# Kernel optimization log

Hardware: AMD Instinct MI355X
Metric: run time of the kernel (lower is better)

The kernel has to match this reference:

```python
import jax, jax.numpy as jnp
import numpy as np

N_NODES = 100000
NFEAT = 256
NHID = 8
HEADS = 8
NCLASS = 32
N_EDGES = 1600000
NEG_SLOPE = 0.2


def setup_inputs() -> dict:
    key = jax.random.key(0)
    ks = jax.random.split(key, 10)
    glorot = lambda k, shape: jax.random.uniform(
        k, shape, jnp.float32, -1.0, 1.0) * np.sqrt(6.0 / (shape[0] + shape[-1]))
    x = jax.random.normal(ks[0], (N_NODES, NFEAT), jnp.float32)
    edge_index = jax.random.randint(ks[1], (2, N_EDGES), 0, N_NODES, jnp.int64)
    W1 = glorot(ks[2], (NFEAT, HEADS * NHID))
    a_src1 = glorot(ks[3], (HEADS, NHID))
    a_dst1 = glorot(ks[4], (HEADS, NHID))
    b1 = jnp.zeros((HEADS * NHID,), jnp.float32)
    W2 = glorot(ks[5], (HEADS * NHID, NCLASS))
    a_src2 = glorot(ks[6], (1, NCLASS))
    a_dst2 = glorot(ks[7], (1, NCLASS))
    b2 = jnp.zeros((NCLASS,), jnp.float32)
    return {"x": x, "edge_index": edge_index, "W1": W1, "a_src1": a_src1,
            "a_dst1": a_dst1, "b1": b1, "W2": W2, "a_src2": a_src2,
            "a_dst2": a_dst2, "b2": b2}


def gat_conv(x, src, dst, W, a_src, a_dst, b, heads, ch, concat):
    """One PyG-style GATConv layer (eval mode, self-loops already in src/dst)."""
    n = x.shape[0]
    h = (x @ W).reshape(n, heads, ch)                      # [N,H,C]
    al_s = jnp.einsum('nhc,hc->nh', h, a_src)              # [N,H]
    al_d = jnp.einsum('nhc,hc->nh', h, a_dst)              # [N,H]
    e = al_s[src] + al_d[dst]                              # [E,H]
    e = jnp.where(e >= 0, e, NEG_SLOPE * e)                # LeakyReLU(0.2)
    # segment softmax over destination node (self-loops => no empty segments)
    m = jax.ops.segment_max(e, dst, num_segments=n)
    e = jnp.exp(e - m[dst])
    s = jax.ops.segment_sum(e, dst, num_segments=n)
    alpha = e / (s[dst] + 1e-16)                           # [E,H]
    msg = h[src] * alpha[:, :, None]                       # [E,H,C]
    out = jax.ops.segment_sum(msg, dst, num_segments=n)    # [N,H,C]
    out = out.reshape(n, heads * ch) if concat else out.mean(axis=1)
    return out + b


def reference(x, edge_index, W1, a_src1, a_dst1, b1, W2, a_src2, a_dst2, b2):
    n = x.shape[0]
    loop = jnp.arange(n, dtype=edge_index.dtype)
    src = jnp.concatenate([edge_index[0], loop])
    dst = jnp.concatenate([edge_index[1], loop])
    h = gat_conv(x, src, dst, W1, a_src1, a_dst1, b1, HEADS, NHID, True)
    h = jax.nn.elu(h)
    out = gat_conv(h, src, dst, W2, a_src2, a_dst2, b2, 1, NCLASS, False)
    return jax.nn.log_softmax(out, axis=1)
```

## Files before the change

kernel.cpp:

```cpp
#include <hip/hip_runtime.h>
#include <math.h>

#define N_NODES 100000
#define NFEAT 256
#define D1 64
#define HEADS 8
#define NHID 8
#define NCLASS 32
#define NUM_EDGES 1600000
#define E_TOT 1700000
#define NEG_SLOPE 0.2f

#define BSHIFT 8
#define NBUCK 391
#define BCAP 5120
#define BIN_EPB 4096
#define BIN_EPT 16
#define GEMM1_NB 1563


#define OFF_H1    0
#define OFF_H2    6400000
#define OFF_ALS1  12800000
#define OFF_ALD1  13600000
#define OFF_ALS2  14400000
#define OFF_ALD2  14500000
#define OFF_BCUR  14600000
#define OFF_ROWP  14601024
#define OFF_CNT   14701024
#define OFF_BIN   14801024
#define OFF_CSR   16802944

typedef __attribute__((ext_vector_type(8))) short bf16x8;
typedef __attribute__((ext_vector_type(4))) float f32x4;

__device__ __forceinline__ float lrelu(float x) { return x >= 0.f ? x : NEG_SLOPE * x; }
__device__ __forceinline__ float fast_elu(float x) { return x > 0.f ? x : __expf(x) - 1.f; }

__device__ __forceinline__ unsigned f32_to_bf16_rne(float f) {
    unsigned u = __float_as_uint(f);
    return (u + 0x7fffu + ((u >> 16) & 1u)) >> 16;
}
__device__ __forceinline__ unsigned pack_bf16x2(float lo, float hi) {
    return f32_to_bf16_rne(lo) | (f32_to_bf16_rne(hi) << 16);
}
__device__ __forceinline__ float2 unpack_bf16x2(unsigned v) {
    return make_float2(__uint_as_float(v << 16), __uint_as_float(v & 0xffff0000u));
}

__device__ __forceinline__ void edge_src_dst(const int* __restrict__ ei, int e, int& src, int& dst) {
    if (e < NUM_EDGES) { src = ei[e]; dst = ei[NUM_EDGES + e]; }
    else { src = e - NUM_EDGES; dst = e - NUM_EDGES; }
}

__global__ __launch_bounds__(256) void bin_kernel(const int* __restrict__ ei,
                                                  int* __restrict__ bcur,
                                                  int* __restrict__ bin) {
    __shared__ int lcnt[NBUCK];
    __shared__ int lbase[NBUCK];
    const int tid = threadIdx.x;
    for (int b = tid; b < NBUCK; b += 256) lcnt[b] = 0;
    __syncthreads();
    const int e0 = blockIdx.x * BIN_EPB;
    int pk[BIN_EPT], bk[BIN_EPT], loff[BIN_EPT];
#pragma unroll
    for (int i = 0; i < BIN_EPT; i++) {
        const int e = e0 + i * 256 + tid;
        if (e < E_TOT) {
            int src, dst; edge_src_dst(ei, e, src, dst);
            bk[i] = dst >> BSHIFT;
            pk[i] = ((dst & 255) << 20) | src;
            loff[i] = atomicAdd(&lcnt[bk[i]], 1);
        } else bk[i] = -1;
    }
    __syncthreads();
    for (int b = tid; b < NBUCK; b += 256) {
        const int c = lcnt[b];
        lbase[b] = c ? atomicAdd(&bcur[b], c) : 0;
    }
    __syncthreads();
#pragma unroll
    for (int i = 0; i < BIN_EPT; i++) {
        if (bk[i] >= 0)
            bin[(size_t)bk[i] * BCAP + lbase[bk[i]] + loff[i]] = pk[i];
    }
}

__global__ __launch_bounds__(256) void gemm1_bsort_kernel(const float* __restrict__ x,
                                                          const float* __restrict__ W1,
                                                          const float* __restrict__ a_src,
                                                          const float* __restrict__ a_dst,
                                                          ushort* __restrict__ h1u,
                                                          float* __restrict__ als,
                                                          float* __restrict__ ald,
                                                          const int* __restrict__ bcur,
                                                          const int* __restrict__ bin,
                                                          int* __restrict__ csr,
                                                          int* __restrict__ row_ptr,
                                                          int* __restrict__ cnt) {
    __shared__ __align__(16) unsigned char smem[23552];
    const int tid = threadIdx.x;

    if (blockIdx.x < NBUCK) {
        int* hcnt = (int*)smem;
        int* hpre = hcnt + 256;
        int* curp = hpre + 256;
        int* ssrc = curp + 256;
        const int bkt = blockIdx.x;
        const int cntb = bcur[bkt];
        const int base = bkt * BCAP;
        hcnt[tid] = 0;
        __syncthreads();
        for (int i = tid; i < cntb; i += 256)
            atomicAdd(&hcnt[bin[base + i] >> 20], 1);
        __syncthreads();
        const int myc = hcnt[tid];
        hpre[tid] = myc;
        __syncthreads();
        for (int off = 1; off < 256; off <<= 1) {
            const int t = (tid >= off) ? hpre[tid - off] : 0;
            __syncthreads();
            hpre[tid] += t;
            __syncthreads();
        }
        const int exc = hpre[tid] - myc;
        curp[tid] = exc;
        __syncthreads();
        for (int i = tid; i < cntb; i += 256) {
            const int v = bin[base + i];
            const int pos = atomicAdd(&curp[v >> 20], 1);
            ssrc[pos] = v & 0xFFFFF;
        }
        __syncthreads();
        for (int i = tid; i < cntb; i += 256) csr[base + i] = ssrc[i];
        const int n = (bkt << BSHIFT) + tid;
        if (n < N_NODES) { row_ptr[n] = base + exc; cnt[n] = myc; }
        return;
    }

    unsigned* xbf = (unsigned*)smem;
    const int wv = tid >> 6;
    const int l = tid & 63;
    const int lm = l & 15;
    const int quad = l >> 4;
    const int r0 = (blockIdx.x - NBUCK) * 64;

    bf16x8 bfrag[8];
#pragma unroll
    for (int kb = 0; kb < 8; kb++)
#pragma unroll
        for (int j = 0; j < 8; j++) {
            const int k = kb * 32 + quad * 8 + j;
            bfrag[kb][j] = (short)f32_to_bf16_rne(W1[k * D1 + wv * 16 + lm]);
        }

    f32x4 acc[4];
#pragma unroll
    for (int s = 0; s < 4; s++) acc[s] = (f32x4)(0.f);

    const int sr = tid >> 2;
    const int sk = (tid & 3) * 8;
    const bool rok = (r0 + sr) < N_NODES;
    const float* xrow = &x[(size_t)(r0 + sr) * NFEAT];
    const int swrd = sr * 20 + (tid & 3) * 4;

    {
        uint4 pv = make_uint4(0, 0, 0, 0);
        if (rok) {
            const float4 va = *(const float4*)&xrow[sk];
            const float4 vb = *(const float4*)&xrow[sk + 4];
            pv.x = pack_bf16x2(va.x, va.y);
            pv.y = pack_bf16x2(va.z, va.w);
            pv.z = pack_bf16x2(vb.x, vb.y);
            pv.w = pack_bf16x2(vb.z, vb.w);
        }
        *(uint4*)&xbf[swrd] = pv;
    }
    __syncthreads();

#pragma unroll
    for (int kb = 0; kb < 8; kb++) {
        const int cur = kb & 1;
        const int nxt = cur ^ 1;
        float4 na = make_float4(0.f, 0.f, 0.f, 0.f);
        float4 nb = make_float4(0.f, 0.f, 0.f, 0.f);
        if (kb < 7 && rok) {
            na = *(const float4*)&xrow[(kb + 1) * 32 + sk];
            nb = *(const float4*)&xrow[(kb + 1) * 32 + sk + 4];
        }
#pragma unroll
        for (int s = 0; s < 4; s++) {
            const uint4 u = *(const uint4*)&xbf[cur * 1280 + (s * 16 + lm) * 20 + quad * 4];
            const bf16x8 af = *(const bf16x8*)&u;
            acc[s] = __builtin_amdgcn_mfma_f32_16x16x32_bf16(af, bfrag[kb], acc[s], 0, 0, 0);
        }
        if (kb < 7) {
            uint4 pv;
            pv.x = pack_bf16x2(na.x, na.y);
            pv.y = pack_bf16x2(na.z, na.w);
            pv.z = pack_bf16x2(nb.x, nb.y);
            pv.w = pack_bf16x2(nb.z, nb.w);
            *(uint4*)&xbf[nxt * 1280 + swrd] = pv;
            __syncthreads();
        }
    }

    const int head = wv * 2 + (lm >> 3);
    const int jc = l & 7;
    const float asl = a_src[head * NHID + jc];
    const float adl = a_dst[head * NHID + jc];
    const int col = wv * 16 + lm;
#pragma unroll
    for (int s = 0; s < 4; s++) {
#pragma unroll
        for (int r = 0; r < 4; r++) {
            const int row = r0 + s * 16 + quad * 4 + r;
            const float v = acc[s][r];
            float ps = v * asl, pd = v * adl;
            ps += __shfl_xor(ps, 1, 64); pd += __shfl_xor(pd, 1, 64);
            ps += __shfl_xor(ps, 2, 64); pd += __shfl_xor(pd, 2, 64);
            ps += __shfl_xor(ps, 4, 64); pd += __shfl_xor(pd, 4, 64);
            if (row < N_NODES) {
                h1u[(size_t)row * D1 + col] = (ushort)f32_to_bf16_rne(v);
                if (jc == 0) { als[row * HEADS + head] = ps; ald[row * HEADS + head] = pd; }
            }
        }
    }
}

__global__ __launch_bounds__(256) void gather1_kernel(const int* __restrict__ row_ptr,
                                                      const int* __restrict__ cnt,
                                                      const int* __restrict__ csr_src,
                                                      const unsigned* __restrict__ h1b,
                                                      const float* __restrict__ als,
                                                      const float* __restrict__ ald,
                                                      const float* __restrict__ b1,
                                                      const float* __restrict__ W2,
                                                      const float* __restrict__ a_src2,
                                                      const float* __restrict__ a_dst2,
                                                      unsigned* __restrict__ h2b,
                                                      float* __restrict__ als2,
                                                      float* __restrict__ ald2) {
    __shared__ float zbuf[4][64];
    const int tid = threadIdx.x;
    const int wv = tid >> 6;
    const int n = blockIdx.x * 4 + wv;
    const int l = tid & 63;
    const int q = l >> 3;
    const int h = l & 7;
    const int start = row_ptr[n];
    const int deg = cnt[n];
    const float aldn = ald[n * HEADS + h];
    float a0 = 0.f, a1 = 0.f, a2 = 0.f, a3 = 0.f;
    float a4 = 0.f, a5 = 0.f, a6 = 0.f, a7 = 0.f, wsum = 0.f;

    int i = q;
    float e0 = 0.f, e1 = 0.f;
    uint4 u0 = make_uint4(0u, 0u, 0u, 0u);
    uint4 u1 = make_uint4(0u, 0u, 0u, 0u);
    int s2 = 0;
    if (i < deg) {
        const int s0 = csr_src[start + i];
        e0 = als[s0 * HEADS + h];
        u0 = *(const uint4*)&h1b[(size_t)s0 * 32 + h * 4];
    }
    if (i + 8 < deg) {
        const int s1 = csr_src[start + i + 8];
        e1 = als[s1 * HEADS + h];
        u1 = *(const uint4*)&h1b[(size_t)s1 * 32 + h * 4];
    }
    if (i + 16 < deg) s2 = csr_src[start + i + 16];

#pragma unroll 2
    for (; i < deg; i += 8) {
        int s3 = 0;
        if (i + 24 < deg) s3 = csr_src[start + i + 24];
        float e2 = 0.f;
        uint4 u2 = make_uint4(0u, 0u, 0u, 0u);
        if (i + 16 < deg) {
            e2 = als[s2 * HEADS + h];
            u2 = *(const uint4*)&h1b[(size_t)s2 * 32 + h * 4];
        }
        const float w = __expf(lrelu(e0 + aldn));
        const float2 p0 = unpack_bf16x2(u0.x);
        const float2 p1 = unpack_bf16x2(u0.y);
        const float2 p2 = unpack_bf16x2(u0.z);
        const float2 p3 = unpack_bf16x2(u0.w);
        a0 = fmaf(p0.x, w, a0); a1 = fmaf(p0.y, w, a1);
        a2 = fmaf(p1.x, w, a2); a3 = fmaf(p1.y, w, a3);
        a4 = fmaf(p2.x, w, a4); a5 = fmaf(p2.y, w, a5);
        a6 = fmaf(p3.x, w, a6); a7 = fmaf(p3.y, w, a7);
        wsum += w;
        e0 = e1; u0 = u1; e1 = e2; u1 = u2; s2 = s3;
    }

    a0 += __shfl_down(a0, 32, 64); a1 += __shfl_down(a1, 32, 64);
    a2 += __shfl_down(a2, 32, 64); a3 += __shfl_down(a3, 32, 64);
    a4 += __shfl_down(a4, 32, 64); a5 += __shfl_down(a5, 32, 64);
    a6 += __shfl_down(a6, 32, 64); a7 += __shfl_down(a7, 32, 64);
    wsum += __shfl_down(wsum, 32, 64);
    a0 += __shfl_down(a0, 16, 64); a1 += __shfl_down(a1, 16, 64);
    a2 += __shfl_down(a2, 16, 64); a3 += __shfl_down(a3, 16, 64);
    a4 += __shfl_down(a4, 16, 64); a5 += __shfl_down(a5, 16, 64);
    a6 += __shfl_down(a6, 16, 64); a7 += __shfl_down(a7, 16, 64);
    wsum += __shfl_down(wsum, 16, 64);
    a0 += __shfl_down(a0, 8, 64); a1 += __shfl_down(a1, 8, 64);
    a2 += __shfl_down(a2, 8, 64); a3 += __shfl_down(a3, 8, 64);
    a4 += __shfl_down(a4, 8, 64); a5 += __shfl_down(a5, 8, 64);
    a6 += __shfl_down(a6, 8, 64); a7 += __shfl_down(a7, 8, 64);
    wsum += __shfl_down(wsum, 8, 64);

    if (l < 8) {
        const float inv = 1.f / (wsum + 1e-16f);
        const float4 b1a = *(const float4*)&b1[l * 8];
        const float4 b1b = *(const float4*)&b1[l * 8 + 4];
        const float z0 = fast_elu(a0 * inv + b1a.x);
        const float z1 = fast_elu(a1 * inv + b1a.y);
        const float z2 = fast_elu(a2 * inv + b1a.z);
        const float z3 = fast_elu(a3 * inv + b1a.w);
        const float z4 = fast_elu(a4 * inv + b1b.x);
        const float z5 = fast_elu(a5 * inv + b1b.y);
        const float z6 = fast_elu(a6 * inv + b1b.z);
        const float z7 = fast_elu(a7 * inv + b1b.w);
        *(float4*)&zbuf[wv][l * 8]     = make_float4(z0, z1, z2, z3);
        *(float4*)&zbuf[wv][l * 8 + 4] = make_float4(z4, z5, z6, z7);
    }
    __builtin_amdgcn_wave_barrier();
    asm volatile("" ::: "memory");

    const int c = l & 31;
    const int kh = l >> 5;
    float y0 = 0.f, y1 = 0.f, y2 = 0.f, y3 = 0.f;
    const float* wbase = &W2[(kh * 32) * NCLASS + c];
#pragma unroll
    for (int j4 = 0; j4 < 2; j4++) {
        const int k0 = j4 * 16;
        const float4 za = *(const float4*)&zbuf[wv][kh * 32 + k0];
        const float4 zb = *(const float4*)&zbuf[wv][kh * 32 + k0 + 4];
        const float4 zc = *(const float4*)&zbuf[wv][kh * 32 + k0 + 8];
        const float4 zd = *(const float4*)&zbuf[wv][kh * 32 + k0 + 12];
        y0 = fmaf(za.x, wbase[(k0 + 0) * NCLASS], y0);
        y1 = fmaf(za.y, wbase[(k0 + 1) * NCLASS], y1);
        y2 = fmaf(za.z, wbase[(k0 + 2) * NCLASS], y2);
        y3 = fmaf(za.w, wbase[(k0 + 3) * NCLASS], y3);
        y0 = fmaf(zb.x, wbase[(k0 + 4) * NCLASS], y0);
        y1 = fmaf(zb.y, wbase[(k0 + 5) * NCLASS], y1);
        y2 = fmaf(zb.z, wbase[(k0 + 6) * NCLASS], y2);
        y3 = fmaf(zb.w, wbase[(k0 + 7) * NCLASS], y3);
        y0 = fmaf(zc.x, wbase[(k0 + 8) * NCLASS], y0);
        y1 = fmaf(zc.y, wbase[(k0 + 9) * NCLASS], y1);
        y2 = fmaf(zc.z, wbase[(k0 + 10) * NCLASS], y2);
        y3 = fmaf(zc.w, wbase[(k0 + 11) * NCLASS], y3);
        y0 = fmaf(zd.x, wbase[(k0 + 12) * NCLASS], y0);
        y1 = fmaf(zd.y, wbase[(k0 + 13) * NCLASS], y1);
        y2 = fmaf(zd.z, wbase[(k0 + 14) * NCLASS], y2);
        y3 = fmaf(zd.w, wbase[(k0 + 15) * NCLASS], y3);
    }
    float y = (y0 + y1) + (y2 + y3);
    y += __shfl_xor(y, 32, 64);

    float part = y * ((l < 32) ? a_src2[c] : a_dst2[c]);
    part += __shfl_xor(part, 1, 64);
    part += __shfl_xor(part, 2, 64);
    part += __shfl_xor(part, 4, 64);
    part += __shfl_xor(part, 8, 64);
    part += __shfl_xor(part, 16, 64);
    const float tdv = __shfl(part, 32, 64);
    if (l == 0) { als2[n] = part; ald2[n] = tdv; }

    const unsigned pw = pack_bf16x2(y, __shfl_down(y, 1, 64));
    if (l < 32 && (l & 1) == 0) h2b[(size_t)n * 16 + (l >> 1)] = pw;
}

__global__ __launch_bounds__(256) void gather2_kernel(const int* __restrict__ row_ptr,
                                                      const int* __restrict__ cnt,
                                                      const int* __restrict__ csr_src,
                                                      const unsigned* __restrict__ h2b,
                                                      const float* __restrict__ als2,
                                                      const float* __restrict__ ald2,
                                                      const float* __restrict__ b2,
                                                      float* __restrict__ out) {
    const int tid = threadIdx.x;
    const int n = blockIdx.x * 4 + (tid >> 6);
    const int l = tid & 63;
    const int q = l >> 2;
    const int c = l & 3;
    const int start = row_ptr[n];
    const int deg = cnt[n];
    const float aldn = ald2[n];
    float a0 = 0.f, a1 = 0.f, a2 = 0.f, a3 = 0.f;
    float a4 = 0.f, a5 = 0.f, a6 = 0.f, a7 = 0.f, wsum = 0.f;

    int i = q;
    float e0 = 0.f, e1 = 0.f;
    uint4 u0 = make_uint4(0u, 0u, 0u, 0u);
    uint4 u1 = make_uint4(0u, 0u, 0u, 0u);
    int s2 = 0;
    if (i < deg) {
        const int s0 = csr_src[start + i];
        e0 = als2[s0];
        u0 = *(const uint4*)&h2b[(size_t)s0 * 16 + c * 4];
    }
    if (i + 16 < deg) {
        const int s1 = csr_src[start + i + 16];
        e1 = als2[s1];
        u1 = *(const uint4*)&h2b[(size_t)s1 * 16 + c * 4];
    }
    if (i + 32 < deg) s2 = csr_src[start + i + 32];

#pragma unroll 2
    for (; i < deg; i += 16) {
        int s3 = 0;
        if (i + 48 < deg) s3 = csr_src[start + i + 48];
        float e2 = 0.f;
        uint4 u2 = make_uint4(0u, 0u, 0u, 0u);
        if (i + 32 < deg) {
            e2 = als2[s2];
            u2 = *(const uint4*)&h2b[(size_t)s2 * 16 + c * 4];
        }
        const float w = __expf(lrelu(e0 + aldn));
        const float2 p0 = unpack_bf16x2(u0.x);
        const float2 p1 = unpack_bf16x2(u0.y);
        const float2 p2 = unpack_bf16x2(u0.z);
        const float2 p3 = unpack_bf16x2(u0.w);
        a0 = fmaf(p0.x, w, a0); a1 = fmaf(p0.y, w, a1);
        a2 = fmaf(p1.x, w, a2); a3 = fmaf(p1.y, w, a3);
        a4 = fmaf(p2.x, w, a4); a5 = fmaf(p2.y, w, a5);
        a6 = fmaf(p3.x, w, a6); a7 = fmaf(p3.y, w, a7);
        wsum += w;
        e0 = e1; u0 = u1; e1 = e2; u1 = u2; s2 = s3;
    }

    a0 += __shfl_down(a0, 32, 64); a1 += __shfl_down(a1, 32, 64);
    a2 += __shfl_down(a2, 32, 64); a3 += __shfl_down(a3, 32, 64);
    a4 += __shfl_down(a4, 32, 64); a5 += __shfl_down(a5, 32, 64);
    a6 += __shfl_down(a6, 32, 64); a7 += __shfl_down(a7, 32, 64);
    wsum += __shfl_down(wsum, 32, 64);
    a0 += __shfl_down(a0, 16, 64); a1 += __shfl_down(a1, 16, 64);
    a2 += __shfl_down(a2, 16, 64); a3 += __shfl_down(a3, 16, 64);
    a4 += __shfl_down(a4, 16, 64); a5 += __shfl_down(a5, 16, 64);
    a6 += __shfl_down(a6, 16, 64); a7 += __shfl_down(a7, 16, 64);
    wsum += __shfl_down(wsum, 16, 64);
    a0 += __shfl_down(a0, 8, 64); a1 += __shfl_down(a1, 8, 64);
    a2 += __shfl_down(a2, 8, 64); a3 += __shfl_down(a3, 8, 64);
    a4 += __shfl_down(a4, 8, 64); a5 += __shfl_down(a5, 8, 64);
    a6 += __shfl_down(a6, 8, 64); a7 += __shfl_down(a7, 8, 64);
    wsum += __shfl_down(wsum, 8, 64);
    a0 += __shfl_down(a0, 4, 64); a1 += __shfl_down(a1, 4, 64);
    a2 += __shfl_down(a2, 4, 64); a3 += __shfl_down(a3, 4, 64);
    a4 += __shfl_down(a4, 4, 64); a5 += __shfl_down(a5, 4, 64);
    a6 += __shfl_down(a6, 4, 64); a7 += __shfl_down(a7, 4, 64);
    wsum += __shfl_down(wsum, 4, 64);

    const float inv = 1.f / (wsum + 1e-16f);
    const float4 b2a = *(const float4*)&b2[c * 8];
    const float4 b2b = *(const float4*)&b2[c * 8 + 4];
    const float v0 = a0 * inv + b2a.x, v1 = a1 * inv + b2a.y;
    const float v2 = a2 * inv + b2a.z, v3 = a3 * inv + b2a.w;
    const float v4 = a4 * inv + b2b.x, v5 = a5 * inv + b2b.y;
    const float v6 = a6 * inv + b2b.z, v7 = a7 * inv + b2b.w;
    float mx = fmaxf(fmaxf(fmaxf(v0, v1), fmaxf(v2, v3)),
                     fmaxf(fmaxf(v4, v5), fmaxf(v6, v7)));
    mx = fmaxf(mx, __shfl_xor(mx, 1, 64));
    mx = fmaxf(mx, __shfl_xor(mx, 2, 64));
    float s = __expf(v0 - mx) + __expf(v1 - mx) + __expf(v2 - mx) + __expf(v3 - mx)
            + __expf(v4 - mx) + __expf(v5 - mx) + __expf(v6 - mx) + __expf(v7 - mx);
    s += __shfl_xor(s, 1, 64);
    s += __shfl_xor(s, 2, 64);
    const float lse = mx + logf(s);
    if (l < 4) {
        float* op = &out[(size_t)n * NCLASS + c * 8];
        *(float4*)&op[0] = make_float4(v0 - lse, v1 - lse, v2 - lse, v3 - lse);
        *(float4*)&op[4] = make_float4(v4 - lse, v5 - lse, v6 - lse, v7 - lse);
    }
}

extern "C" void kernel_launch(void* const* d_in, const int* in_sizes, int n_in,
                              void* d_out, int out_size, void* d_ws, size_t ws_size,
                              hipStream_t stream) {
    const float* x      = (const float*)d_in[0];
    const int*   ei     = (const int*)d_in[1];
    const float* W1     = (const float*)d_in[2];
    const float* a_src1 = (const float*)d_in[3];
    const float* a_dst1 = (const float*)d_in[4];
    const float* b1     = (const float*)d_in[5];
    const float* W2     = (const float*)d_in[6];
    const float* a_src2 = (const float*)d_in[7];
    const float* a_dst2 = (const float*)d_in[8];
    const float* b2     = (const float*)d_in[9];
    float* out = (float*)d_out;
    float* ws  = (float*)d_ws;

    ushort* h1u     = (ushort*)(ws + OFF_H1);
    unsigned* h1b   = (unsigned*)(ws + OFF_H1);
    unsigned* h2b   = (unsigned*)(ws + OFF_H2);
    float* als1     = ws + OFF_ALS1;
    float* ald1     = ws + OFF_ALD1;
    float* als2     = ws + OFF_ALS2;
    float* ald2     = ws + OFF_ALD2;
    int*   bcur     = (int*)(ws + OFF_BCUR);
    int*   row_ptr  = (int*)(ws + OFF_ROWP);
    int*   cnt      = (int*)(ws + OFF_CNT);
    int*   bin      = (int*)(ws + OFF_BIN);
    int*   csr      = (int*)(ws + OFF_CSR);

    hipMemsetAsync(bcur, 0, NBUCK * sizeof(int), stream);

    bin_kernel<<<(E_TOT + BIN_EPB - 1) / BIN_EPB, 256, 0, stream>>>(ei, bcur, bin);
    gemm1_bsort_kernel<<<NBUCK + GEMM1_NB, 256, 0, stream>>>(x, W1, a_src1, a_dst1,
                                                             h1u, als1, ald1,
                                                             bcur, bin, csr, row_ptr, cnt);
    gather1_kernel<<<N_NODES / 4, 256, 0, stream>>>(row_ptr, cnt, csr, h1b, als1, ald1,
                                                    b1, W2, a_src2, a_dst2, h2b, als2, ald2);
    gather2_kernel<<<N_NODES / 4, 256, 0, stream>>>(row_ptr, cnt, csr, h2b, als2, ald2, b2, out);
}
```

Measured before the change: 329.4 us.

## Pad CSR rows to multiples of 16 with sentinel node to drop gather bounds checks

Each destination's CSR segment is padded up to a multiple of 16 entries, filled with a sentinel source index whose features are zero and whose attention logit is -inf, so padded edges contribute zero weight. The gather loops for both layers then drop the per-iteration degree predicates and load unconditionally, clamping prefetch offsets instead. The bucket sort now scatters directly to global memory rather than staging through shared memory, which shrinks LDS use. The cost is a larger CSR buffer, extra padded work per node (up to 15 wasted edges), and uncoalesced global writes during the sort.

Measured after the change: 345.3 us. 1.05x slower.

```diff
diff --git a/kernel.cpp b/kernel.cpp
--- a/kernel.cpp
+++ b/kernel.cpp
@@ -10,10 +10,12 @@
 #define NUM_EDGES 1600000
 #define E_TOT 1700000
 #define NEG_SLOPE 0.2f
+#define SENT N_NODES
 
 #define BSHIFT 8
 #define NBUCK 391
-#define BCAP 5120
+#define BCAP_BIN 5120
+#define BCAP_CSR 8192
 #define BIN_EPB 4096
 #define BIN_EPT 16
 #define GEMM1_NB 1563
@@ -22,14 +24,14 @@
 #define OFF_H1    0
 #define OFF_H2    6400000
 #define OFF_ALS1  12800000
-#define OFF_ALD1  13600000
-#define OFF_ALS2  14400000
-#define OFF_ALD2  14500000
-#define OFF_BCUR  14600000
-#define OFF_ROWP  14601024
-#define OFF_CNT   14701024
-#define OFF_BIN   14801024
-#define OFF_CSR   16802944
+#define OFF_ALD1  13700000
+#define OFF_ALS2  14600000
+#define OFF_ALD2  14800000
+#define OFF_BCUR  15000000
+#define OFF_ROWP  15001024
+#define OFF_CNT   15101024
+#define OFF_BIN   15201024
+#define OFF_CSR   17202944
 
 typedef __attribute__((ext_vector_type(8))) short bf16x8;
 typedef __attribute__((ext_vector_type(4))) float f32x4;
@@ -82,7 +84,7 @@
 #pragma unroll
     for (int i = 0; i < BIN_EPT; i++) {
         if (bk[i] >= 0)
-            bin[(size_t)bk[i] * BCAP + lbase[bk[i]] + loff[i]] = pk[i];
+            bin[(size_t)bk[i] * BCAP_BIN + lbase[bk[i]] + loff[i]] = pk[i];
     }
 }
 
@@ -98,24 +100,25 @@
                                                           int* __restrict__ csr,
                                                           int* __restrict__ row_ptr,
                                                           int* __restrict__ cnt) {
-    __shared__ __align__(16) unsigned char smem[23552];
+    __shared__ __align__(16) unsigned char smem[10240];
     const int tid = threadIdx.x;
 
     if (blockIdx.x < NBUCK) {
         int* hcnt = (int*)smem;
         int* hpre = hcnt + 256;
         int* curp = hpre + 256;
-        int* ssrc = curp + 256;
         const int bkt = blockIdx.x;
         const int cntb = bcur[bkt];
-        const int base = bkt * BCAP;
+        const int base5 = bkt * BCAP_BIN;
+        const int base8 = bkt * BCAP_CSR;
         hcnt[tid] = 0;
         __syncthreads();
         for (int i = tid; i < cntb; i += 256)
-            atomicAdd(&hcnt[bin[base + i] >> 20], 1);
+            atomicAdd(&hcnt[bin[base5 + i] >> 20], 1);
         __syncthreads();
         const int myc = hcnt[tid];
-        hpre[tid] = myc;
+        const int rc = (myc + 15) & ~15;
+        hpre[tid] = rc;
         __syncthreads();
         for (int off = 1; off < 256; off <<= 1) {
             const int t = (tid >= off) ? hpre[tid - off] : 0;
@@ -123,18 +126,17 @@
             hpre[tid] += t;
             __syncthreads();
         }
-        const int exc = hpre[tid] - myc;
+        const int exc = hpre[tid] - rc;
         curp[tid] = exc;
         __syncthreads();
         for (int i = tid; i < cntb; i += 256) {
-            const int v = bin[base + i];
+            const int v = bin[base5 + i];
             const int pos = atomicAdd(&curp[v >> 20], 1);
-            ssrc[pos] = v & 0xFFFFF;
-        }
-        __syncthreads();
-        for (int i = tid; i < cntb; i += 256) csr[base + i] = ssrc[i];
+            csr[base8 + pos] = v & 0xFFFFF;
+        }
+        for (int j = exc + myc; j < exc + rc; j++) csr[base8 + j] = SENT;
         const int n = (bkt << BSHIFT) + tid;
-        if (n < N_NODES) { row_ptr[n] = base + exc; cnt[n] = myc; }
+        if (n < N_NODES) { row_ptr[n] = base8 + exc; cnt[n] = rc; }
         return;
     }
 
@@ -144,6 +146,11 @@
     const int lm = l & 15;
     const int quad = l >> 4;
     const int r0 = (blockIdx.x - NBUCK) * 64;
+
+    if (r0 == 0) {
+        if (tid < 32) ((unsigned*)h1u)[(size_t)SENT * 32 + tid] = 0u;
+        else if (tid < 40) als[(size_t)SENT * HEADS + (tid - 32)] = -INFINITY;
+    }
 
     bf16x8 bfrag[8];
 #pragma unroll
@@ -248,50 +255,44 @@
     const int l = tid & 63;
     const int q = l >> 3;
     const int h = l & 7;
+
+    if (blockIdx.x == 0 && wv == 0) {
+        if (l < 16) h2b[(size_t)SENT * 16 + l] = 0u;
+        else if (l == 16) als2[SENT] = -INFINITY;
+    }
+
     const int start = row_ptr[n];
-    const int deg = cnt[n];
+    const int dpad = cnt[n];
     const float aldn = ald[n * HEADS + h];
     float a0 = 0.f, a1 = 0.f, a2 = 0.f, a3 = 0.f;
     float a4 = 0.f, a5 = 0.f, a6 = 0.f, a7 = 0.f, wsum = 0.f;
 
     int i = q;
-    float e0 = 0.f, e1 = 0.f;
-    uint4 u0 = make_uint4(0u, 0u, 0u, 0u);
-    uint4 u1 = make_uint4(0u, 0u, 0u, 0u);
-    int s2 = 0;
-    if (i < deg) {
-        const int s0 = csr_src[start + i];
-        e0 = als[s0 * HEADS + h];
-        u0 = *(const uint4*)&h1b[(size_t)s0 * 32 + h * 4];
-    }
-    if (i + 8 < deg) {
-        const int s1 = csr_src[start + i + 8];
-        e1 = als[s1 * HEADS + h];
-        u1 = *(const uint4*)&h1b[(size_t)s1 * 32 + h * 4];
-    }
-    if (i + 16 < deg) s2 = csr_src[start + i + 16];
-
-#pragma unroll 2
-    for (; i < deg; i += 8) {
-        int s3 = 0;
-        if (i + 24 < deg) s3 = csr_src[start + i + 24];
-        float e2 = 0.f;
-        uint4 u2 = make_uint4(0u, 0u, 0u, 0u);
-        if (i + 16 < deg) {
-            e2 = als[s2 * HEADS + h];
-            u2 = *(const uint4*)&h1b[(size_t)s2 * 32 + h * 4];
-        }
-        const float w = __expf(lrelu(e0 + aldn));
-        const float2 p0 = unpack_bf16x2(u0.x);
-        const float2 p1 = unpack_bf16x2(u0.y);
-        const float2 p2 = unpack_bf16x2(u0.z);
-        const float2 p3 = unpack_bf16x2(u0.w);
+    const int sA0 = csr_src[start + i];
+    const int sB0 = csr_src[start + i + 8];
+    int o2 = i + 16; o2 = (o2 < dpad) ? o2 : q;
+    int sC = csr_src[start + o2];
+    float eA = als[sA0 * HEADS + h];
+    uint4 uA = *(const uint4*)&h1b[(size_t)sA0 * 32 + h * 4];
+    float eB = als[sB0 * HEADS + h];
+    uint4 uB = *(const uint4*)&h1b[(size_t)sB0 * 32 + h * 4];
+
+    for (; i < dpad; i += 8) {
+        int o3 = i + 24; o3 = (o3 < dpad) ? o3 : q;
+        const int sD = csr_src[start + o3];
+        const float eC = als[sC * HEADS + h];
+        const uint4 uC = *(const uint4*)&h1b[(size_t)sC * 32 + h * 4];
+        const float w = __expf(lrelu(eA + aldn));
+        const float2 p0 = unpack_bf16x2(uA.x);
+        const float2 p1 = unpack_bf16x2(uA.y);
+        const float2 p2 = unpack_bf16x2(uA.z);
+        const float2 p3 = unpack_bf16x2(uA.w);
         a0 = fmaf(p0.x, w, a0); a1 = fmaf(p0.y, w, a1);
         a2 = fmaf(p1.x, w, a2); a3 = fmaf(p1.y, w, a3);
         a4 = fmaf(p2.x, w, a4); a5 = fmaf(p2.y, w, a5);
         a6 = fmaf(p3.x, w, a6); a7 = fmaf(p3.y, w, a7);
         wsum += w;
-        e0 = e1; u0 = u1; e1 = e2; u1 = u2; s2 = s3;
+        eA = eB; uA = uB; eB = eC; uB = uC; sC = sD;
     }
 
     a0 += __shfl_down(a0, 32, 64); a1 += __shfl_down(a1, 32, 64);
@@ -386,49 +387,38 @@
     const int q = l >> 2;
     const int c = l & 3;
     const int start = row_ptr[n];
-    const int deg = cnt[n];
+    const int dpad = cnt[n];
     const float aldn = ald2[n];
     float a0 = 0.f, a1 = 0.f, a2 = 0.f, a3 = 0.f;
     float a4 = 0.f, a5 = 0.f, a6 = 0.f, a7 = 0.f, wsum = 0.f;
 
     int i = q;
-    float e0 = 0.f, e1 = 0.f;
-    uint4 u0 = make_uint4(0u, 0u, 0u, 0u);
-    uint4 u1 = make_uint4(0u, 0u, 0u, 0u);
-    int s2 = 0;
-    if (i < deg) {
-        const int s0 = csr_src[start + i];
-        e0 = als2[s0];
-        u0 = *(const uint4*)&h2b[(size_t)s0 * 16 + c * 4];
-    }
-    if (i + 16 < deg) {
-        const int s1 = csr_src[start + i + 16];
-        e1 = als2[s1];
-        u1 = *(const uint4*)&h2b[(size_t)s1 * 16 + c * 4];
-    }
-    if (i + 32 < deg) s2 = csr_src[start + i + 32];
-
-#pragma unroll 2
-    for (; i < deg; i += 16) {
-        int s3 = 0;
-        if (i + 48 < deg) s3 = csr_src[start + i + 48];
-        float e2 = 0.f;
-        uint4 u2 = make_uint4(0u, 0u, 0u, 0u);
-        if (i + 32 < deg) {
-            e2 = als2[s2];
-            u2 = *(const uint4*)&h2b[(size_t)s2 * 16 + c * 4];
-        }
-        const float w = __expf(lrelu(e0 + aldn));
-        const float2 p0 = unpack_bf16x2(u0.x);
-        const float2 p1 = unpack_bf16x2(u0.y);
-        const float2 p2 = unpack_bf16x2(u0.z);
-        const float2 p3 = unpack_bf16x2(u0.w);
+    const int sA0 = csr_src[start + i];
+    int o1 = i + 16; o1 = (o1 < dpad) ? o1 : q;
+    int sC = csr_src[start + o1];
+    float eA = als2[sA0];
+    uint4 uA = *(const uint4*)&h2b[(size_t)sA0 * 16 + c * 4];
+    float eB = als2[sC];
+    uint4 uB = *(const uint4*)&h2b[(size_t)sC * 16 + c * 4];
+    int o2 = i + 32; o2 = (o2 < dpad) ? o2 : q;
+    sC = csr_src[start + o2];
+
+    for (; i < dpad; i += 16) {
+        int o3 = i + 48; o3 = (o3 < dpad) ? o3 : q;
+        const int sD = csr_src[start + o3];
+        const float eC = als2[sC];
+        const uint4 uC = *(const uint4*)&h2b[(size_t)sC * 16 + c * 4];
+        const float w = __expf(lrelu(eA + aldn));
+        const float2 p0 = unpack_bf16x2(uA.x);
+        const float2 p1 = unpack_bf16x2(uA.y);
+        const float2 p2 = unpack_bf16x2(uA.z);
+        const float2 p3 = unpack_bf16x2(uA.w);
         a0 = fmaf(p0.x, w, a0); a1 = fmaf(p0.y, w, a1);
         a2 = fmaf(p1.x, w, a2); a3 = fmaf(p1.y, w, a3);
         a4 = fmaf(p2.x, w, a4); a5 = fmaf(p2.y, w, a5);
         a6 = fmaf(p3.x, w, a6); a7 = fmaf(p3.y, w, a7);
         wsum += w;
-        e0 = e1; u0 = u1; e1 = e2; u1 = u2; s2 = s3;
+        eA = eB; uA = uB; eB = eC; uB = uC; sC = sD;
     }
 
     a0 += __shfl_down(a0, 32, 64); a1 += __shfl_down(a1, 32, 64);
```
